# Kernel optimization log

Measured on AMD Instinct MI355X. Metric: run time of the kernel, lower is better.

## Reference

```python
import jax, jax.numpy as jnp
import numpy as np

K = 8192      # infeatures
N = 28672     # outfeatures
R = 64        # EoRA rank
PACK = 8      # 4-bit values per int32


def setup_inputs() -> dict:
    key = jax.random.key(0)
    ks = jax.random.split(key, 7)
    x = jax.random.normal(ks[0], (1, K), dtype=jnp.float32)
    qweight = jax.random.randint(ks[1], (K // PACK, N), jnp.iinfo(jnp.int32).min,
                                 jnp.iinfo(jnp.int32).max, dtype=jnp.int32)
    # per-output-channel quant params (zeros is pre-multiplied scale*zero, GPTQ-style)
    scales = (jax.random.uniform(ks[2], (1, N), dtype=jnp.float32) * 0.01 + 0.001)
    zeros = scales * (7.5 + jax.random.uniform(ks[3], (1, N), dtype=jnp.float32))
    bias = jax.random.normal(ks[4], (N,), dtype=jnp.float32)
    down = (jax.random.normal(ks[5], (K, R), dtype=jnp.float32) * 0.02).astype(jnp.float16)
    up = (jax.random.normal(ks[6], (R, N), dtype=jnp.float32) * 0.02).astype(jnp.float16)
    return {"x": x, "qweight": qweight, "scales": scales, "zeros": zeros,
            "bias": bias, "down": down, "up": up}


def _dequant4(qweight, scales, zeros):
    # unpack 8 nibbles per int32 along the input dim: (K//8, N) -> (K, N)
    shifts = (jnp.arange(PACK, dtype=jnp.int32) * 4)
    q = (qweight[:, None, :] >> shifts[None, :, None]) & 0xF  # (K//8, 8, N)
    q = q.reshape(-1, qweight.shape[-1]).astype(jnp.float32)  # (K, N)
    return scales * q - zeros  # broadcast (1,N) over rows


def reference(x, qweight, scales, zeros, bias, up, down):
    dtype = x.dtype
    xf = x.astype(jnp.float32)          # x = x.float()
    xh = xf.astype(jnp.float16)         # xh = x.half()
    # int4 dequantized matvec: y = bias + xf @ W_deq   (fp32 accumulation)
    W = _dequant4(qweight, scales, zeros)               # (K, N) fp32
    y = bias + (xf @ W)[0]                              # (N,)
    # EoRA low-rank correction in fp16
    down_proj = xh @ down                               # (1, R) fp16
    corr = (down_proj @ up).reshape(-1)                 # (N,) fp16
    y = y + corr                                        # fp32 + fp16 -> fp32
    return y.astype(dtype).reshape(1, N)
```

## Files before the change

### kernel.cpp

```cpp
#include <hip/hip_runtime.h>
#include <hip/hip_fp16.h>


#define KDIM 8192
#define NDIM 28672
#define RDIM 64

#define KCHUNKS 64
#define KPC (KDIM / KCHUNKS)
#define KBPC (KPC / 8)
#define CPB 1024
#define NBLK (NDIM / CPB)

#define PB 8
#define PKPB (KDIM / PB)

#define QPART_FLOATS (KCHUNKS * NDIM)
#define DP_OFF QPART_FLOATS
#define WS_NEED ((QPART_FLOATS + PB * RDIM) * 4)

__global__ __launch_bounds__(256, 8) void quant_kernel(const float* __restrict__ x,
                                                       const int* __restrict__ qw,
                                                       const float* __restrict__ scales,
                                                       const float* __restrict__ zeros,
                                                       const float* __restrict__ bias,
                                                       const float* __restrict__ down,
                                                       float* __restrict__ ws) {
    const int t  = threadIdx.x;
    const int ph = blockIdx.y;

    if (ph < KCHUNKS) {
        const int n0 = blockIdx.x * CPB + t * 4;
        __shared__ __align__(16) float xs[KPC];
        __shared__ float sxs;
        if (t < KPC / 4) {
            *(float4*)&xs[t * 4] = *(const float4*)&x[ph * KPC + t * 4];
        }
        __syncthreads();
        if (t < 64) {
            float s = xs[t * 2] + xs[t * 2 + 1];
            #pragma unroll
            for (int o = 32; o >= 1; o >>= 1) s += __shfl_down(s, o, 64);
            if (t == 0) sxs = s;
        }
        __syncthreads();
        const float Sxc = sxs;

        float a0 = 0.f, a1 = 0.f, a2 = 0.f, a3 = 0.f;
        const int* qp = qw + (size_t)(ph * KBPC) * NDIM + n0;
        for (int g = 0; g < KBPC; g += 4) {
            int4 v[4];
            #pragma unroll
            for (int u = 0; u < 4; ++u) {
                v[u] = *(const int4*)(qp + (size_t)(g + u) * NDIM);
            }
            #pragma unroll
            for (int u = 0; u < 4; ++u) {
                const unsigned wx = (unsigned)v[u].x, wy = (unsigned)v[u].y;
                const unsigned wz = (unsigned)v[u].z, ww = (unsigned)v[u].w;
                const float* xr = &xs[(g + u) * 8];
                #pragma unroll
                for (int j = 0; j < 8; ++j) {
                    const float xj = xr[j];
                    a0 = fmaf(xj, (float)((wx >> (4 * j)) & 0xFu), a0);
                    a1 = fmaf(xj, (float)((wy >> (4 * j)) & 0xFu), a1);
                    a2 = fmaf(xj, (float)((wz >> (4 * j)) & 0xFu), a2);
                    a3 = fmaf(xj, (float)((ww >> (4 * j)) & 0xFu), a3);
                }
            }
        }

        const float4 sc = *(const float4*)&scales[n0];
        const float4 zr = *(const float4*)&zeros[n0];
        float4 p;
        p.x = fmaf(sc.x, a0, -zr.x * Sxc);
        p.y = fmaf(sc.y, a1, -zr.y * Sxc);
        p.z = fmaf(sc.z, a2, -zr.z * Sxc);
        p.w = fmaf(sc.w, a3, -zr.w * Sxc);
        if (ph == 0) {
            const float4 bi = *(const float4*)&bias[n0];
            p.x += bi.x; p.y += bi.y; p.z += bi.z; p.w += bi.w;
        }
        *(float4*)&ws[(size_t)ph * NDIM + n0] = p;
    } else if (blockIdx.x < PB) {
        const int b = blockIdx.x;
        const int w = t >> 6;
        const int l = t & 63;
        const int grp = l >> 4;
        const int li = l & 15;

        __shared__ float xsp[PKPB];
        {
            float4 v = *(const float4*)&x[b * PKPB + t * 4];
            v.x = __half2float(__float2half(v.x));
            v.y = __half2float(__float2half(v.y));
            v.z = __half2float(__float2half(v.z));
            v.w = __half2float(__float2half(v.w));
            *(float4*)&xsp[t * 4] = v;
        }
        __syncthreads();

        const float* dbase = down + (size_t)b * PKPB * RDIM;
        float a0 = 0.f, a1 = 0.f, a2 = 0.f, a3 = 0.f;
        for (int i = 0; i < 64; i += 4) {
            float4 v[4];
            #pragma unroll
            for (int u = 0; u < 4; ++u) {
                const int q = (i + u) * 4 + w;
                v[u] = *(const float4*)&dbase[(size_t)q * 256 + l * 4];
            }
            #pragma unroll
            for (int u = 0; u < 4; ++u) {
                const int q = (i + u) * 4 + w;
                const float xv = xsp[q * 4 + grp];
                a0 = fmaf(xv, v[u].x, a0);
                a1 = fmaf(xv, v[u].y, a1);
                a2 = fmaf(xv, v[u].z, a2);
                a3 = fmaf(xv, v[u].w, a3);
            }
        }

        a0 += __shfl_xor(a0, 16, 64); a0 += __shfl_xor(a0, 32, 64);
        a1 += __shfl_xor(a1, 16, 64); a1 += __shfl_xor(a1, 32, 64);
        a2 += __shfl_xor(a2, 16, 64); a2 += __shfl_xor(a2, 32, 64);
        a3 += __shfl_xor(a3, 16, 64); a3 += __shfl_xor(a3, 32, 64);

        __shared__ float part[4][RDIM];
        if (l < 16) {
            part[w][li * 4 + 0] = a0;
            part[w][li * 4 + 1] = a1;
            part[w][li * 4 + 2] = a2;
            part[w][li * 4 + 3] = a3;
        }
        __syncthreads();
        if (t < RDIM) {
            ws[DP_OFF + b * RDIM + t] =
                part[0][t] + part[1][t] + part[2][t] + part[3][t];
        }
    }
}

__global__ __launch_bounds__(256) void reduce_kernel(const float* __restrict__ ws,
                                                     const float* __restrict__ upf,
                                                     float* __restrict__ out) {
    const int t = threadIdx.x;
    const int n = blockIdx.x * 256 + t;

    __shared__ float dps[RDIM];
    if (t < RDIM) {
        float d = 0.f;
        #pragma unroll
        for (int b = 0; b < PB; ++b) d += ws[DP_OFF + b * RDIM + t];
        dps[t] = __half2float(__float2half(d));
    }
    __syncthreads();

    float acc = 0.f;
    #pragma unroll 16
    for (int ph = 0; ph < KCHUNKS; ++ph) {
        acc += ws[(size_t)ph * NDIM + n];
    }
    float e = 0.f;
    #pragma unroll 8
    for (int r = 0; r < RDIM; ++r) {
        e = fmaf(dps[r], upf[(size_t)r * NDIM + n], e);
    }
    out[n] = acc + e;
}

__global__ __launch_bounds__(256) void fused_fallback(const float* __restrict__ x,
                                                      const int* __restrict__ qw,
                                                      const float* __restrict__ scales,
                                                      const float* __restrict__ zeros,
                                                      const float* __restrict__ bias,
                                                      const float* __restrict__ down,
                                                      const float* __restrict__ up,
                                                      float* __restrict__ out) {
    const int t  = threadIdx.x;
    const int ph = blockIdx.y;
    const int n0 = blockIdx.x * CPB + t * 4;

    if (ph < KCHUNKS) {
        __shared__ __align__(16) float xs[KPC];
        __shared__ float sxs;
        if (t < KPC / 4) {
            *(float4*)&xs[t * 4] = *(const float4*)&x[ph * KPC + t * 4];
        }
        __syncthreads();
        if (t < 64) {
            float s = xs[t * 2] + xs[t * 2 + 1];
            #pragma unroll
            for (int o = 32; o >= 1; o >>= 1) s += __shfl_down(s, o, 64);
            if (t == 0) sxs = s;
        }
        __syncthreads();
        const float Sxc = sxs;
        float a0 = 0.f, a1 = 0.f, a2 = 0.f, a3 = 0.f;
        const int* qp = qw + (size_t)(ph * KBPC) * NDIM + n0;
        for (int kb = 0; kb < KBPC; ++kb) {
            const int4 wv = *(const int4*)qp;
            qp += NDIM;
            const unsigned wx = (unsigned)wv.x, wy = (unsigned)wv.y;
            const unsigned wz = (unsigned)wv.z, ww = (unsigned)wv.w;
            const float* xr = &xs[kb * 8];
            #pragma unroll
            for (int j = 0; j < 8; ++j) {
                const float xj = xr[j];
                a0 = fmaf(xj, (float)((wx >> (4 * j)) & 0xFu), a0);
                a1 = fmaf(xj, (float)((wy >> (4 * j)) & 0xFu), a1);
                a2 = fmaf(xj, (float)((wz >> (4 * j)) & 0xFu), a2);
                a3 = fmaf(xj, (float)((ww >> (4 * j)) & 0xFu), a3);
            }
        }
        const float4 sc = *(const float4*)&scales[n0];
        const float4 zr = *(const float4*)&zeros[n0];
        float p0 = fmaf(sc.x, a0, -zr.x * Sxc);
        float p1 = fmaf(sc.y, a1, -zr.y * Sxc);
        float p2 = fmaf(sc.z, a2, -zr.z * Sxc);
        float p3 = fmaf(sc.w, a3, -zr.w * Sxc);
        if (ph == 0) {
            const float4 bi = *(const float4*)&bias[n0];
            p0 += bi.x; p1 += bi.y; p2 += bi.z; p3 += bi.w;
        }
        atomicAdd(&out[n0 + 0], p0);
        atomicAdd(&out[n0 + 1], p1);
        atomicAdd(&out[n0 + 2], p2);
        atomicAdd(&out[n0 + 3], p3);
    } else {
        const int r  = t & 63;
        const int w  = t >> 6;
        const int k0 = w * (KDIM / 4);
        float acc0 = 0.f, acc1 = 0.f;
        for (int k = k0; k < k0 + KDIM / 4; k += 2) {
            const float xv0 = __half2float(__float2half(x[k]));
            const float xv1 = __half2float(__float2half(x[k + 1]));
            acc0 = fmaf(xv0, down[(size_t)k * RDIM + r], acc0);
            acc1 = fmaf(xv1, down[(size_t)(k + 1) * RDIM + r], acc1);
        }
        __shared__ float part[4][64];
        part[w][r] = acc0 + acc1;
        __syncthreads();
        __shared__ float dp[RDIM];
        if (t < 64) {
            const float d = part[0][t] + part[1][t] + part[2][t] + part[3][t];
            dp[t] = __half2float(__float2half(d));
        }
        __syncthreads();
        float e0 = 0.f, e1 = 0.f, e2 = 0.f, e3 = 0.f;
        #pragma unroll 8
        for (int rr = 0; rr < RDIM; ++rr) {
            const float d = dp[rr];
            const float4 uv = *(const float4*)&up[(size_t)rr * NDIM + n0];
            e0 = fmaf(d, uv.x, e0);
            e1 = fmaf(d, uv.y, e1);
            e2 = fmaf(d, uv.z, e2);
            e3 = fmaf(d, uv.w, e3);
        }
        atomicAdd(&out[n0 + 0], e0);
        atomicAdd(&out[n0 + 1], e1);
        atomicAdd(&out[n0 + 2], e2);
        atomicAdd(&out[n0 + 3], e3);
    }
}

extern "C" void kernel_launch(void* const* d_in, const int* in_sizes, int n_in,
                              void* d_out, int out_size, void* d_ws, size_t ws_size,
                              hipStream_t stream) {
    const float* x      = (const float*)d_in[0];
    const int*   qw     = (const int*)d_in[1];
    const float* scales = (const float*)d_in[2];
    const float* zeros  = (const float*)d_in[3];
    const float* bias   = (const float*)d_in[4];
    const float* down   = (const float*)d_in[5];
    const float* up     = (const float*)d_in[6];
    float* out = (float*)d_out;
    float* ws  = (float*)d_ws;

    if (ws_size >= WS_NEED) {
        quant_kernel<<<dim3(NBLK, KCHUNKS + 1), 256, 0, stream>>>(
            x, qw, scales, zeros, bias, down, ws);
        reduce_kernel<<<NDIM / 256, 256, 0, stream>>>(ws, up, out);
    } else {
        hipMemsetAsync(out, 0, (size_t)NDIM * sizeof(float), stream);
        fused_fallback<<<dim3(NBLK, KCHUNKS + 1), 256, 0, stream>>>(
            x, qw, scales, zeros, bias, down, up, out);
    }
}
```

Before: 35.51 us.

## Dequantize int4 via fp16 magic-number trick and packed fdot2 accumulation

Replaces the per-nibble shift/convert/fma sequence with a trick: masking nibble pairs and ORing with 0x6400 yields fp16 values 1024+q. These are multiplied against fp16-packed x using v_dot2 with fp32 accumulation, and the 1024*sum(x) bias is removed afterwards. The first weight tile is loaded before the shared-memory setup and barrier, and the k loop is fully unrolled. This cuts ALU instructions per weight, but x is now rounded to fp16 in the quantized matvec. That changes numerics against the fp32 reference, and subtracting 1024*Sx from large accumulators risks cancellation error.

New measurement: 32.22 us. 1.1x faster.

```diff
diff --git a/kernel.cpp b/kernel.cpp
--- a/kernel.cpp
+++ b/kernel.cpp
@@ -18,6 +18,19 @@
 #define QPART_FLOATS (KCHUNKS * NDIM)
 #define DP_OFF QPART_FLOATS
 #define WS_NEED ((QPART_FLOATS + PB * RDIM) * 4)
+
+typedef _Float16 h2v __attribute__((ext_vector_type(2)));
+
+__device__ __forceinline__ float dot2p(unsigned up, unsigned xp, float acc) {
+#if __has_builtin(__builtin_amdgcn_fdot2)
+    return __builtin_amdgcn_fdot2(__builtin_bit_cast(h2v, up),
+                                  __builtin_bit_cast(h2v, xp), acc, false);
+#else
+    h2v a = __builtin_bit_cast(h2v, up);
+    h2v b = __builtin_bit_cast(h2v, xp);
+    return acc + (float)a.x * (float)b.x + (float)a.y * (float)b.y;
+#endif
+}
 
 __global__ __launch_bounds__(256, 8) void quant_kernel(const float* __restrict__ x,
                                                        const int* __restrict__ qw,
@@ -31,52 +44,96 @@
 
     if (ph < KCHUNKS) {
         const int n0 = blockIdx.x * CPB + t * 4;
-        __shared__ __align__(16) float xs[KPC];
+        const int* qp = qw + (size_t)(ph * KBPC) * NDIM + n0;
+
+        int4 v0[4];
+        #pragma unroll
+        for (int u = 0; u < 4; ++u) {
+            v0[u] = *(const int4*)(qp + (size_t)u * NDIM);
+        }
+
+        __shared__ unsigned xsp[KBPC * 4];
         __shared__ float sxs;
-        if (t < KPC / 4) {
-            *(float4*)&xs[t * 4] = *(const float4*)&x[ph * KPC + t * 4];
-        }
-        __syncthreads();
-        if (t < 64) {
-            float s = xs[t * 2] + xs[t * 2 + 1];
-            #pragma unroll
-            for (int o = 32; o >= 1; o >>= 1) s += __shfl_down(s, o, 64);
+        if (t < KBPC) {
+            const int base = ph * KPC + t * 8;
+            const float4 f0 = *(const float4*)&x[base];
+            const float4 f1 = *(const float4*)&x[base + 4];
+            h2v p0 = { (_Float16)f0.x, (_Float16)f1.x };
+            h2v p1 = { (_Float16)f0.y, (_Float16)f1.y };
+            h2v p2 = { (_Float16)f0.z, (_Float16)f1.z };
+            h2v p3 = { (_Float16)f0.w, (_Float16)f1.w };
+            xsp[t * 4 + 0] = __builtin_bit_cast(unsigned, p0);
+            xsp[t * 4 + 1] = __builtin_bit_cast(unsigned, p1);
+            xsp[t * 4 + 2] = __builtin_bit_cast(unsigned, p2);
+            xsp[t * 4 + 3] = __builtin_bit_cast(unsigned, p3);
+            float s = (float)p0.x + (float)p0.y + (float)p1.x + (float)p1.y +
+                      (float)p2.x + (float)p2.y + (float)p3.x + (float)p3.y;
+            s += __shfl_down(s, 8, 16);
+            s += __shfl_down(s, 4, 16);
+            s += __shfl_down(s, 2, 16);
+            s += __shfl_down(s, 1, 16);
             if (t == 0) sxs = s;
         }
         __syncthreads();
-        const float Sxc = sxs;
+        const float Sxh = sxs;
+
+        const unsigned M = 0x000F000Fu;
+        const unsigned E = 0x64006400u;
 
         float a0 = 0.f, a1 = 0.f, a2 = 0.f, a3 = 0.f;
-        const int* qp = qw + (size_t)(ph * KBPC) * NDIM + n0;
-        for (int g = 0; g < KBPC; g += 4) {
+
+        #define CONSUME(vv, g)                                                \
+        {                                                                     \
+            _Pragma("unroll")                                                 \
+            for (int u = 0; u < 4; ++u) {                                     \
+                const int row = (g) * 4 + u;                                  \
+                const unsigned xp0 = xsp[row * 4 + 0];                        \
+                const unsigned xp1 = xsp[row * 4 + 1];                        \
+                const unsigned xp2 = xsp[row * 4 + 2];                        \
+                const unsigned xp3 = xsp[row * 4 + 3];                        \
+                const unsigned wx = (unsigned)vv[u].x;                        \
+                const unsigned wy = (unsigned)vv[u].y;                        \
+                const unsigned wz = (unsigned)vv[u].z;                        \
+                const unsigned ww = (unsigned)vv[u].w;                        \
+                a0 = dot2p((wx & M) | E, xp0, a0);                            \
+                a0 = dot2p(((wx >> 4) & M) | E, xp1, a0);                     \
+                a0 = dot2p(((wx >> 8) & M) | E, xp2, a0);                     \
+                a0 = dot2p(((wx >> 12) & M) | E, xp3, a0);                    \
+                a1 = dot2p((wy & M) | E, xp0, a1);                            \
+                a1 = dot2p(((wy >> 4) & M) | E, xp1, a1);                     \
+                a1 = dot2p(((wy >> 8) & M) | E, xp2, a1);                     \
+                a1 = dot2p(((wy >> 12) & M) | E, xp3, a1);                    \
+                a2 = dot2p((wz & M) | E, xp0, a2);                            \
+                a2 = dot2p(((wz >> 4) & M) | E, xp1, a2);                     \
+                a2 = dot2p(((wz >> 8) & M) | E, xp2, a2);                     \
+                a2 = dot2p(((wz >> 12) & M) | E, xp3, a2);                    \
+                a3 = dot2p((ww & M) | E, xp0, a3);                            \
+                a3 = dot2p(((ww >> 4) & M) | E, xp1, a3);                     \
+                a3 = dot2p(((ww >> 8) & M) | E, xp2, a3);                     \
+                a3 = dot2p(((ww >> 12) & M) | E, xp3, a3);                    \
+            }                                                                 \
+        }
+
+        CONSUME(v0, 0);
+        #pragma unroll
+        for (int g = 1; g < KBPC / 4; ++g) {
             int4 v[4];
             #pragma unroll
             for (int u = 0; u < 4; ++u) {
-                v[u] = *(const int4*)(qp + (size_t)(g + u) * NDIM);
+                v[u] = *(const int4*)(qp + (size_t)(g * 4 + u) * NDIM);
             }
-            #pragma unroll
-            for (int u = 0; u < 4; ++u) {
-                const unsigned wx = (unsigned)v[u].x, wy = (unsigned)v[u].y;
-                const unsigned wz = (unsigned)v[u].z, ww = (unsigned)v[u].w;
-                const float* xr = &xs[(g + u) * 8];
-                #pragma unroll
-                for (int j = 0; j < 8; ++j) {
-                    const float xj = xr[j];
-                    a0 = fmaf(xj, (float)((wx >> (4 * j)) & 0xFu), a0);
-                    a1 = fmaf(xj, (float)((wy >> (4 * j)) & 0xFu), a1);
-                    a2 = fmaf(xj, (float)((wz >> (4 * j)) & 0xFu), a2);
-                    a3 = fmaf(xj, (float)((ww >> (4 * j)) & 0xFu), a3);
-                }
-            }
-        }
+            CONSUME(v, g);
+        }
+        #undef CONSUME
 
         const float4 sc = *(const float4*)&scales[n0];
         const float4 zr = *(const float4*)&zeros[n0];
+        const float corr = 1024.f * Sxh;
         float4 p;
-        p.x = fmaf(sc.x, a0, -zr.x * Sxc);
-        p.y = fmaf(sc.y, a1, -zr.y * Sxc);
-        p.z = fmaf(sc.z, a2, -zr.z * Sxc);
-        p.w = fmaf(sc.w, a3, -zr.w * Sxc);
+        p.x = fmaf(sc.x, a0 - corr, -zr.x * Sxh);
+        p.y = fmaf(sc.y, a1 - corr, -zr.y * Sxh);
+        p.z = fmaf(sc.z, a2 - corr, -zr.z * Sxh);
+        p.w = fmaf(sc.w, a3 - corr, -zr.w * Sxh);
         if (ph == 0) {
             const float4 bi = *(const float4*)&bias[n0];
             p.x += bi.x; p.y += bi.y; p.z += bi.z; p.w += bi.w;
@@ -89,14 +146,14 @@
         const int grp = l >> 4;
         const int li = l & 15;
 
-        __shared__ float xsp[PKPB];
+        __shared__ float xsp2[PKPB];
         {
             float4 v = *(const float4*)&x[b * PKPB + t * 4];
             v.x = __half2float(__float2half(v.x));
             v.y = __half2float(__float2half(v.y));
             v.z = __half2float(__float2half(v.z));
             v.w = __half2float(__float2half(v.w));
-            *(float4*)&xsp[t * 4] = v;
+            *(float4*)&xsp2[t * 4] = v;
         }
         __syncthreads();
 
@@ -112,7 +169,7 @@
             #pragma unroll
             for (int u = 0; u < 4; ++u) {
                 const int q = (i + u) * 4 + w;
-                const float xv = xsp[q * 4 + grp];
+                const float xv = xsp2[q * 4 + grp];
                 a0 = fmaf(xv, v[u].x, a0);
                 a1 = fmaf(xv, v[u].y, a1);
                 a2 = fmaf(xv, v[u].z, a2);
```
